# Performance work log

Hardware: AMD Instinct MI355X
Metric: run time of the kernel (lower is better)

Reference implementation:

```python
import jax, jax.numpy as jnp
import numpy as np

NUM_HEADS = 16
NUM_KV_HEADS = 4
HEAD_DIM = 64
HIDDEN = 1024
B, S = 2, 2048


def setup_inputs() -> dict:
    key = jax.random.key(0)
    ks = jax.random.split(key, 9)
    sc = 0.02
    return {
        "x": jax.random.normal(ks[0], (B, S, HIDDEN), dtype=jnp.float32),
        "Wq": jax.random.normal(ks[1], (HIDDEN, NUM_HEADS * HEAD_DIM), dtype=jnp.float32) * sc,
        "bq": jnp.zeros((NUM_HEADS * HEAD_DIM,), dtype=jnp.float32),
        "Wk": jax.random.normal(ks[2], (HIDDEN, NUM_KV_HEADS * HEAD_DIM), dtype=jnp.float32) * sc,
        "bk": jnp.zeros((NUM_KV_HEADS * HEAD_DIM,), dtype=jnp.float32),
        "Wv": jax.random.normal(ks[3], (HIDDEN, NUM_KV_HEADS * HEAD_DIM), dtype=jnp.float32) * sc,
        "bv": jnp.zeros((NUM_KV_HEADS * HEAD_DIM,), dtype=jnp.float32),
        "Wo": jax.random.normal(ks[4], (NUM_HEADS * HEAD_DIM, HIDDEN), dtype=jnp.float32) * sc,
        "bo": jnp.zeros((HIDDEN,), dtype=jnp.float32),
    }


def reference(x, Wq, bq, Wk, bk, Wv, bv, Wo, bo):
    bs, seq, _ = x.shape
    groups = NUM_HEADS // NUM_KV_HEADS
    # projections -> [B, H, S, D]
    q = (x @ Wq + bq).reshape(bs, seq, NUM_HEADS, HEAD_DIM).transpose(0, 2, 1, 3)
    k = (x @ Wk + bk).reshape(bs, seq, NUM_KV_HEADS, HEAD_DIM).transpose(0, 2, 1, 3)
    v = (x @ Wv + bv).reshape(bs, seq, NUM_KV_HEADS, HEAD_DIM).transpose(0, 2, 1, 3)
    # repeat_interleave KV heads to match query heads (GQA expansion)
    k = jnp.repeat(k, groups, axis=1)
    v = jnp.repeat(v, groups, axis=1)
    # NOTE: source applies NO 1/sqrt(d) scaling and no mask/ALiBi
    scores = jnp.einsum("bhqd,bhkd->bhqk", q, k)
    attn = jax.nn.softmax(scores.astype(jnp.float32), axis=-1).astype(q.dtype)
    out = jnp.einsum("bhqk,bhkd->bhqd", attn, v)
    out = out.transpose(0, 2, 1, 3).reshape(bs, seq, NUM_HEADS * HEAD_DIM)
    return out @ Wo + bo
```

## Files before the change

### kernel.cpp

```cpp
#include <hip/hip_runtime.h>

#define NHEADS 16
#define NKV    4
#define HDIM   64
#define HIDDEN 1024
#define BATCH  2
#define SEQ    2048
#define MROWS  (BATCH * SEQ)
#define LOG2E  1.44269504088896340736f

typedef __bf16 bf16_t;
typedef bf16_t bf16x8 __attribute__((ext_vector_type(8)));
typedef float  f32x4  __attribute__((ext_vector_type(4)));

__device__ __forceinline__ float bf2f(unsigned short u) {
    return __uint_as_float(((unsigned int)u) << 16);
}
__device__ __forceinline__ unsigned short f2bf(float f) {
    unsigned int u = __float_as_uint(f);
    u += 0x7FFFu + ((u >> 16) & 1u);
    return (unsigned short)(u >> 16);
}

__device__ __forceinline__ void gld16(const unsigned short* g, unsigned short* l)
{
    __builtin_amdgcn_global_load_lds(
        (const __attribute__((address_space(1))) void*)g,
        (__attribute__((address_space(3))) void*)l,
        16, 0, 0);
}

__device__ __forceinline__ int swz(int row, int ch) {
    return (row * 8 + (ch ^ (row & 7))) * 8;
}

__device__ __forceinline__ bool sniff_is_f32(const unsigned short* __restrict__ x)
{
    const int e = (x[threadIdx.x & 63] >> 7) & 0xFF;
    const unsigned long long ok = __ballot(e >= 110 && e <= 140);
    return __popcll(ok) < 56;
}

__device__ __forceinline__ void load8cvt(const void* base, size_t elem, bool isf32, unsigned short out[8])
{
    if (!isf32) {
        *(uint4*)out = *(const uint4*)((const unsigned short*)base + elem);
    } else {
        const float* p = (const float*)base + elem;
        float4 v0 = *(const float4*)p;
        float4 v1 = *(const float4*)(p + 4);
        out[0] = f2bf(v0.x); out[1] = f2bf(v0.y); out[2] = f2bf(v0.z); out[3] = f2bf(v0.w);
        out[4] = f2bf(v1.x); out[5] = f2bf(v1.y); out[6] = f2bf(v1.z); out[7] = f2bf(v1.w);
    }
}
__device__ __forceinline__ float bias_at(const void* b, int i, bool isf32)
{
    return isf32 ? ((const float*)b)[i] : bf2f(((const unsigned short*)b)[i]);
}

__global__ __launch_bounds__(256)
void prep_kernel(const void* __restrict__ x,
                 const void* __restrict__ Wq, const void* __restrict__ Wk,
                 const void* __restrict__ Wv, const void* __restrict__ Wo,
                 unsigned short* __restrict__ xb,
                 unsigned short* __restrict__ Wqkvt,
                 unsigned short* __restrict__ Wot)
{
    const bool isf32 = sniff_is_f32((const unsigned short*)x);
    const int t = threadIdx.x;
    int bid = blockIdx.x;

    if (bid < 2048) {
        if (!isf32) return;
        const size_t c = (size_t)bid * 256 + t;
        unsigned short v[8];
        load8cvt(x, c * 8, true, v);
        *(uint4*)(&xb[c * 8]) = *(uint4*)v;
        return;
    }
    bid -= 2048;
    const void* src; unsigned short* dst; int N, rowoff;
    if (bid < 256)      {             src = Wq; dst = Wqkvt; N = 1024; rowoff = 0;    }
    else if (bid < 320) { bid -= 256; src = Wk; dst = Wqkvt; N = 256;  rowoff = 1024; }
    else if (bid < 384) { bid -= 320; src = Wv; dst = Wqkvt; N = 256;  rowoff = 1280; }
    else                { bid -= 384; src = Wo; dst = Wot;   N = 1024; rowoff = 0;    }
    const int ntx = N / 64;
    const int gn0 = (bid % ntx) * 64;
    const int gk0 = (bid / ntx) * 64;

    __shared__ unsigned short Ts[64][72];
#pragma unroll
    for (int half = 0; half < 2; ++half) {
        const int kl = (t >> 3) + half * 32;
        const int n8 = (t & 7) * 8;
        unsigned short v[8];
        load8cvt(src, (size_t)(gk0 + kl) * N + gn0 + n8, isf32, v);
        *(uint4*)(&Ts[kl][n8]) = *(uint4*)v;
    }
    __syncthreads();
#pragma unroll
    for (int half = 0; half < 2; ++half) {
        const int nl = (t >> 3) + half * 32;
        const int k8 = (t & 7) * 8;
        unsigned short v[8];
#pragma unroll
        for (int j = 0; j < 8; ++j) v[j] = Ts[k8 + j][nl];
        *(uint4*)(&dst[(size_t)(rowoff + gn0 + nl) * HIDDEN + gk0 + k8]) = *(uint4*)v;
    }
}

template<int TBM, int TBN, int KK>
__device__ __forceinline__ void gemm_tile(const unsigned short* __restrict__ A,
                                          const unsigned short* __restrict__ Bt,
                                          int m0, int n0,
                                          unsigned short* As, unsigned short* Bs,
                                          f32x4 (&acc)[TBM / 32][TBN / 32])
{
    const int tid  = threadIdx.x;
    const int lane = tid & 63;
    const int wave = tid >> 6;
    const int quad = lane >> 4;
    const int l15  = lane & 15;
    const int wr   = wave >> 1;
    const int wc   = wave & 1;

    const int srow = tid >> 3;
    const int gch  = ((tid & 7) ^ (srow & 7)) * 8;

    const unsigned short* ga[TBM / 32];
    const unsigned short* gb[TBN / 32];
#pragma unroll
    for (int r = 0; r < TBM / 32; ++r)
        ga[r] = A + (size_t)(m0 + srow + r * 32) * KK + gch;
#pragma unroll
    for (int r = 0; r < TBN / 32; ++r)
        gb[r] = Bt + (size_t)(n0 + srow + r * 32) * KK + gch;

    const int ldw = wave * 512;

    int aoffs[2][TBM / 32], boffs[2][TBN / 32];
#pragma unroll
    for (int kk = 0; kk < 2; ++kk) {
#pragma unroll
        for (int i = 0; i < TBM / 32; ++i)
            aoffs[kk][i] = swz(wr * (TBM / 2) + i * 16 + l15, kk * 4 + quad);
#pragma unroll
        for (int j = 0; j < TBN / 32; ++j)
            boffs[kk][j] = swz(wc * (TBN / 2) + j * 16 + l15, kk * 4 + quad);
    }

#define GEMM_STAGE(buf)                                                         \
    do {                                                                        \
        _Pragma("unroll")                                                       \
        for (int r = 0; r < TBM / 32; ++r) {                                    \
            gld16(ga[r], &As[(buf) * TBM * 64 + r * 2048 + ldw]);               \
            ga[r] += 64;                                                        \
        }                                                                       \
        _Pragma("unroll")                                                       \
        for (int r = 0; r < TBN / 32; ++r) {                                    \
            gld16(gb[r], &Bs[(buf) * TBN * 64 + r * 2048 + ldw]);               \
            gb[r] += 64;                                                        \
        }                                                                       \
    } while (0)

    constexpr int nk = KK / 64;
    GEMM_STAGE(0);
#pragma unroll
    for (int k = 0; k < nk; ++k) {
        const int cur = k & 1;
        __syncthreads();
        if (k + 1 < nk) GEMM_STAGE(cur ^ 1);

#pragma unroll
        for (int kk = 0; kk < 2; ++kk) {
            bf16x8 af[TBM / 32], bfv[TBN / 32];
#pragma unroll
            for (int i = 0; i < TBM / 32; ++i)
                af[i] = *(const bf16x8*)(&As[cur * TBM * 64 + aoffs[kk][i]]);
#pragma unroll
            for (int j = 0; j < TBN / 32; ++j)
                bfv[j] = *(const bf16x8*)(&Bs[cur * TBN * 64 + boffs[kk][j]]);
            __builtin_amdgcn_s_setprio(1);
#pragma unroll
            for (int i = 0; i < TBM / 32; ++i)
#pragma unroll
                for (int j = 0; j < TBN / 32; ++j)
                    acc[i][j] = __builtin_amdgcn_mfma_f32_16x16x32_bf16(af[i], bfv[j], acc[i][j], 0, 0, 0);
            __builtin_amdgcn_s_setprio(0);
        }
    }
#undef GEMM_STAGE
}

__global__ __launch_bounds__(256)
void gemm_qkv(const void* __restrict__ xraw,
              const unsigned short* __restrict__ xb,
              const unsigned short* __restrict__ Bt,
              const void* __restrict__ bq, const void* __restrict__ bk,
              const void* __restrict__ bv,
              unsigned short* __restrict__ Qh,
              unsigned short* __restrict__ Kh,
              unsigned short* __restrict__ Vt)
{
    __shared__ __align__(16) unsigned short As[2 * 128 * 64];
    __shared__ __align__(16) unsigned short Bs[2 * 64 * 64];
    const bool bias_f32 = sniff_is_f32((const unsigned short*)xraw);
    const unsigned short* A = bias_f32 ? xb : (const unsigned short*)xraw;
    const int lane = threadIdx.x & 63;
    const int wave = threadIdx.x >> 6;
    const int quad = lane >> 4, l15 = lane & 15;
    const int wr = wave >> 1, wc = wave & 1;
    const int m0 = blockIdx.y * 128, n0 = blockIdx.x * 64;

    f32x4 acc[4][2] = {};
    gemm_tile<128, 64, HIDDEN>(A, Bt, m0, n0, As, Bs, acc);

#pragma unroll
    for (int i = 0; i < 4; ++i) {
#pragma unroll
        for (int j = 0; j < 2; ++j) {
            const int nn  = n0 + wc * 32 + j * 16 + l15;
            const int mmb = m0 + wr * 64 + i * 16 + quad * 4;
            const int b = mmb >> 11, s0 = mmb & 2047;
            if (nn < 1024) {
                const float bias = bias_at(bq, nn, bias_f32);
                const int h = nn >> 6, d = nn & 63;
                const size_t idx0 = (((size_t)(b * NHEADS + h)) * SEQ + s0) * 64 + d;
#pragma unroll
                for (int r = 0; r < 4; ++r)
                    Qh[idx0 + (size_t)r * 64] = f2bf((acc[i][j][r] + bias) * LOG2E);
            } else if (nn < 1280) {
                const int nk = nn - 1024;
                const float bias = bias_at(bk, nk, bias_f32);
                const int h = nk >> 6, d = nk & 63;
                const size_t idx0 = (((size_t)(b * NKV + h)) * SEQ + s0) * 64 + d;
#pragma unroll
                for (int r = 0; r < 4; ++r)
                    Kh[idx0 + (size_t)r * 64] = f2bf(acc[i][j][r] + bias);
            } else {
                const int nv = nn - 1280;
                const float bias = bias_at(bv, nv, bias_f32);
                const int h = nv >> 6, d = nv & 63;
                const size_t idx = (((size_t)(b * NKV + h)) * 64 + d) * SEQ + s0;
                unsigned short vv[4];
#pragma unroll
                for (int r = 0; r < 4; ++r) vv[r] = f2bf(acc[i][j][r] + bias);
                *(uint2*)(&Vt[idx]) = *(uint2*)vv;
            }
        }
    }
}

__global__ __launch_bounds__(256)
void gemm_o(const void* __restrict__ xraw,
            const unsigned short* __restrict__ A,
            const unsigned short* __restrict__ Bt,
            const void* __restrict__ bo,
            float* __restrict__ out)
{
    __shared__ __align__(16) unsigned short As[2 * 128 * 64];
    __shared__ __align__(16) unsigned short Bs[2 * 64 * 64];
    const bool bias_f32 = sniff_is_f32((const unsigned short*)xraw);
    const int lane = threadIdx.x & 63;
    const int wave = threadIdx.x >> 6;
    const int quad = lane >> 4, l15 = lane & 15;
    const int wr = wave >> 1, wc = wave & 1;
    const int m0 = blockIdx.y * 128, n0 = blockIdx.x * 64;

    f32x4 acc[4][2] = {};
    gemm_tile<128, 64, HIDDEN>(A, Bt, m0, n0, As, Bs, acc);

#pragma unroll
    for (int i = 0; i < 4; ++i) {
#pragma unroll
        for (int j = 0; j < 2; ++j) {
            const int nn = n0 + wc * 32 + j * 16 + l15;
            const float bvv = bias_at(bo, nn, bias_f32);
#pragma unroll
            for (int r = 0; r < 4; ++r) {
                const int mm = m0 + wr * 64 + i * 16 + quad * 4 + r;
                out[(size_t)mm * HIDDEN + nn] = acc[i][j][r] + bvv;
            }
        }
    }
}

#define PLD   72
#define NT    (SEQ / 64)
#define KVOFF (64 * 64)

__global__ __launch_bounds__(256)
void attn_kernel(const unsigned short* __restrict__ Qh,
                 const unsigned short* __restrict__ Kh,
                 const unsigned short* __restrict__ Vt,
                 unsigned short* __restrict__ O)
{
    __shared__ __align__(16) unsigned short Kth[2 * KVOFF];
    __shared__ __align__(16) unsigned short VtT[2 * KVOFF];
    __shared__ __align__(16) unsigned short Pt[4 * 32 * PLD];

    const int tid  = threadIdx.x;
    const int lane = tid & 63;
    const int wave = tid >> 6;
    const int quad = lane >> 4;
    const int l15  = lane & 15;

    const int qt = blockIdx.x;
    const int h  = blockIdx.y;
    const int b  = blockIdx.z;
    const int kv = h >> 2;

    const size_t qoff = ((size_t)(b * NHEADS + h)) * SEQ * HDIM;
    const size_t koff = ((size_t)(b * NKV + kv)) * SEQ * HDIM;
    const size_t voff = ((size_t)(b * NKV + kv)) * HDIM * SEQ;

    const int q0 = qt * 128 + wave * 32;

    bf16x8 qf0[2], qf1[2];
#pragma unroll
    for (int qs = 0; qs < 2; ++qs) {
        const size_t qrow = qoff + (size_t)(q0 + qs * 16 + l15) * HDIM;
        qf0[qs] = *(const bf16x8*)(&Qh[qrow + quad * 8]);
        qf1[qs] = *(const bf16x8*)(&Qh[qrow + 32 + quad * 8]);
    }

    bf16x8 onesv;
#pragma unroll
    for (int i = 0; i < 8; ++i) onesv[i] = (bf16_t)1.0f;

    f32x4 o0[4] = {}, o1[4] = {};
    f32x4 lacc0 = {}, lacc1 = {};

    int koff0[4], koff1[4], pw[2][4], prd[2], voffs[2][4];
#pragma unroll
    for (int j = 0; j < 4; ++j) {
        koff0[j] = swz(j * 16 + l15, quad);
        koff1[j] = swz(j * 16 + l15, quad ^ 4);
        pw[0][j] = wave * 32 * PLD + l15 * PLD + j * 16 + quad * 4;
        pw[1][j] = pw[0][j] + 16 * PLD;
    }
#pragma unroll
    for (int kk = 0; kk < 2; ++kk) {
        prd[kk] = wave * 32 * PLD + l15 * PLD + kk * 32 + quad * 8;
#pragma unroll
        for (int dt = 0; dt < 4; ++dt)
            voffs[kk][dt] = swz(dt * 16 + l15, kk * 4 + quad);
    }

    const unsigned short* kp = Kh + koff;
    const unsigned short* vp = Vt + voff;
    const int srow0 = tid >> 3;
    const int gch_s = ((tid & 7) ^ (srow0 & 7)) * 8;

#define ATTN_STAGE(buf)                                                          \
    do {                                                                         \
        gld16(kp + (size_t)srow0 * HDIM + gch_s,        &Kth[(buf)*KVOFF + wave * 512]);        \
        gld16(kp + (size_t)(srow0 + 32) * HDIM + gch_s, &Kth[(buf)*KVOFF + 2048 + wave * 512]); \
        gld16(vp + (size_t)srow0 * SEQ + gch_s,         &VtT[(buf)*KVOFF + wave * 512]);        \
        gld16(vp + (size_t)(srow0 + 32) * SEQ + gch_s,  &VtT[(buf)*KVOFF + 2048 + wave * 512]); \
        kp += 64 * HDIM; vp += 64;                                               \
    } while (0)

    ATTN_STAGE(0);

#pragma unroll 2
    for (int kt = 0; kt < NT; ++kt) {
        const int cur = kt & 1;
        __syncthreads();
        if (kt + 1 < NT) ATTN_STAGE(cur ^ 1);

#pragma unroll
        for (int j = 0; j < 4; ++j) {
            const bf16x8 kh0 = *(const bf16x8*)(&Kth[cur * KVOFF + koff0[j]]);
            const bf16x8 kh1 = *(const bf16x8*)(&Kth[cur * KVOFF + koff1[j]]);
#pragma unroll
            for (int qs = 0; qs < 2; ++qs) {
                f32x4 z = {};
                __builtin_amdgcn_s_setprio(1);
                z = __builtin_amdgcn_mfma_f32_16x16x32_bf16(kh0, qs ? qf0[1] : qf0[0], z, 0, 0, 0);
                const f32x4 sc = __builtin_amdgcn_mfma_f32_16x16x32_bf16(kh1, qs ? qf1[1] : qf1[0], z, 0, 0, 0);
                __builtin_amdgcn_s_setprio(0);
                const float p0 = __builtin_amdgcn_exp2f(sc[0]);
                const float p1 = __builtin_amdgcn_exp2f(sc[1]);
                const float p2 = __builtin_amdgcn_exp2f(sc[2]);
                const float p3 = __builtin_amdgcn_exp2f(sc[3]);
                uint2 w;
                w.x = __builtin_amdgcn_perm(__float_as_uint(p1), __float_as_uint(p0), 0x07060302u);
                w.y = __builtin_amdgcn_perm(__float_as_uint(p3), __float_as_uint(p2), 0x07060302u);
                *(uint2*)(&Pt[pw[qs][j]]) = w;
            }
        }

#pragma unroll
        for (int kk = 0; kk < 2; ++kk) {
            const bf16x8 pf0 = *(const bf16x8*)(&Pt[prd[kk]]);
            const bf16x8 pf1 = *(const bf16x8*)(&Pt[prd[kk] + 16 * PLD]);
            __builtin_amdgcn_s_setprio(1);
            lacc0 = __builtin_amdgcn_mfma_f32_16x16x32_bf16(onesv, pf0, lacc0, 0, 0, 0);
            lacc1 = __builtin_amdgcn_mfma_f32_16x16x32_bf16(onesv, pf1, lacc1, 0, 0, 0);
#pragma unroll
            for (int dt = 0; dt < 4; ++dt) {
                const bf16x8 vf = *(const bf16x8*)(&VtT[cur * KVOFF + voffs[kk][dt]]);
                o0[dt] = __builtin_amdgcn_mfma_f32_16x16x32_bf16(vf, pf0, o0[dt], 0, 0, 0);
                o1[dt] = __builtin_amdgcn_mfma_f32_16x16x32_bf16(vf, pf1, o1[dt], 0, 0, 0);
            }
            __builtin_amdgcn_s_setprio(0);
        }
    }
#undef ATTN_STAGE

#pragma unroll
    for (int qs = 0; qs < 2; ++qs) {
        const float inv = 1.0f / (qs ? lacc1[0] : lacc0[0]);
        const size_t rowbase = ((size_t)b * SEQ + (q0 + qs * 16 + l15)) * (NHEADS * HDIM) + h * HDIM;
#pragma unroll
        for (int dt = 0; dt < 4; ++dt) {
            const f32x4 ov = qs ? o1[dt] : o0[dt];
            unsigned short v4[4];
#pragma unroll
            for (int r = 0; r < 4; ++r) v4[r] = f2bf(ov[r] * inv);
            *(uint2*)(&O[rowbase + dt * 16 + quad * 4]) = *(uint2*)v4;
        }
    }
}

extern "C" void kernel_launch(void* const* d_in, const int* in_sizes, int n_in,
                              void* d_out, int out_size, void* d_ws, size_t ws_size,
                              hipStream_t stream)
{
    const void* x  = d_in[0];
    const void* Wq = d_in[1];
    const void* bq = d_in[2];
    const void* Wk = d_in[3];
    const void* bk = d_in[4];
    const void* Wv = d_in[5];
    const void* bv = d_in[6];
    const void* Wo = d_in[7];
    const void* bo = d_in[8];
    float* out = (float*)d_out;

    unsigned short* p = (unsigned short*)d_ws;
    unsigned short* xb    = p; p += (size_t)MROWS * HIDDEN;
    unsigned short* Wqkvt = p; p += (size_t)1536 * HIDDEN;
    unsigned short* Wot   = p; p += (size_t)HIDDEN * HIDDEN;
    unsigned short* Qh = p;  p += (size_t)MROWS * 1024;
    unsigned short* Kh = p;  p += (size_t)2 * NKV * SEQ * HDIM;
    unsigned short* Vt = p;  p += (size_t)2 * NKV * SEQ * HDIM;
    unsigned short* A2 = p;  p += (size_t)MROWS * 1024;

    dim3 blk(256);
    prep_kernel<<<dim3(2688), blk, 0, stream>>>(x, Wq, Wk, Wv, Wo, xb, Wqkvt, Wot);
    gemm_qkv<<<dim3(1536 / 64, MROWS / 128), blk, 0, stream>>>(
        x, xb, Wqkvt, bq, bk, bv, Qh, Kh, Vt);
    attn_kernel<<<dim3(SEQ / 128, NHEADS, BATCH), blk, 0, stream>>>(Qh, Kh, Vt, A2);
    gemm_o<<<dim3(1024 / 64, MROWS / 128), blk, 0, stream>>>(x, A2, Wot, bo, out);
}
```

Before: 176.5 us.

## Triple-buffer GEMM and attention loads with explicit vmcnt waits, shrink GEMM tiles

```diff
diff --git a/kernel.cpp b/kernel.cpp
--- a/kernel.cpp
+++ b/kernel.cpp
@@ -12,6 +12,9 @@
 typedef __bf16 bf16_t;
 typedef bf16_t bf16x8 __attribute__((ext_vector_type(8)));
 typedef float  f32x4  __attribute__((ext_vector_type(4)));
+
+template<int N>  struct ic { static constexpr int  v = N; };
+template<bool B> struct bc { static constexpr bool v = B; };
 
 __device__ __forceinline__ float bf2f(unsigned short u) {
     return __uint_as_float(((unsigned int)u) << 16);
@@ -109,13 +112,14 @@
     }
 }
 
-template<int TBM, int TBN, int KK>
+template<int KK>
 __device__ __forceinline__ void gemm_tile(const unsigned short* __restrict__ A,
                                           const unsigned short* __restrict__ Bt,
                                           int m0, int n0,
                                           unsigned short* As, unsigned short* Bs,
-                                          f32x4 (&acc)[TBM / 32][TBN / 32])
-{
+                                          f32x4 (&acc)[2][2])
+{
+    static_assert(KK / 64 == 16, "pipeline schedule assumes 16 K-steps");
     const int tid  = threadIdx.x;
     const int lane = tid & 63;
     const int wave = tid >> 6;
@@ -127,69 +131,75 @@
     const int srow = tid >> 3;
     const int gch  = ((tid & 7) ^ (srow & 7)) * 8;
 
-    const unsigned short* ga[TBM / 32];
-    const unsigned short* gb[TBN / 32];
-#pragma unroll
-    for (int r = 0; r < TBM / 32; ++r)
-        ga[r] = A + (size_t)(m0 + srow + r * 32) * KK + gch;
-#pragma unroll
-    for (int r = 0; r < TBN / 32; ++r)
+    const unsigned short* ga[2];
+    const unsigned short* gb[2];
+#pragma unroll
+    for (int r = 0; r < 2; ++r) {
+        ga[r] = A  + (size_t)(m0 + srow + r * 32) * KK + gch;
         gb[r] = Bt + (size_t)(n0 + srow + r * 32) * KK + gch;
-
-    const int ldw = wave * 512;
-
-    int aoffs[2][TBM / 32], boffs[2][TBN / 32];
+    }
+    unsigned short* const adst = As + wave * 512;
+    unsigned short* const bdst = Bs + wave * 512;
+
+    int aoffs[2][2], boffs[2][2];
 #pragma unroll
     for (int kk = 0; kk < 2; ++kk) {
 #pragma unroll
-        for (int i = 0; i < TBM / 32; ++i)
-            aoffs[kk][i] = swz(wr * (TBM / 2) + i * 16 + l15, kk * 4 + quad);
-#pragma unroll
-        for (int j = 0; j < TBN / 32; ++j)
-            boffs[kk][j] = swz(wc * (TBN / 2) + j * 16 + l15, kk * 4 + quad);
-    }
-
-#define GEMM_STAGE(buf)                                                         \
-    do {                                                                        \
-        _Pragma("unroll")                                                       \
-        for (int r = 0; r < TBM / 32; ++r) {                                    \
-            gld16(ga[r], &As[(buf) * TBM * 64 + r * 2048 + ldw]);               \
-            ga[r] += 64;                                                        \
-        }                                                                       \
-        _Pragma("unroll")                                                       \
-        for (int r = 0; r < TBN / 32; ++r) {                                    \
-            gld16(gb[r], &Bs[(buf) * TBN * 64 + r * 2048 + ldw]);               \
-            gb[r] += 64;                                                        \
-        }                                                                       \
+        for (int i = 0; i < 2; ++i) {
+            aoffs[kk][i] = swz(wr * 32 + i * 16 + l15, kk * 4 + quad);
+            boffs[kk][i] = swz(wc * 32 + i * 16 + l15, kk * 4 + quad);
+        }
+    }
+
+#define GSTAGE(B)                                                \
+    do {                                                         \
+        gld16(ga[0], adst + (B) * 4096);        ga[0] += 64;     \
+        gld16(ga[1], adst + (B) * 4096 + 2048); ga[1] += 64;     \
+        gld16(gb[0], bdst + (B) * 4096);        gb[0] += 64;     \
+        gld16(gb[1], bdst + (B) * 4096 + 2048); gb[1] += 64;     \
     } while (0)
 
-    constexpr int nk = KK / 64;
-    GEMM_STAGE(0);
-#pragma unroll
-    for (int k = 0; k < nk; ++k) {
-        const int cur = k & 1;
-        __syncthreads();
-        if (k + 1 < nk) GEMM_STAGE(cur ^ 1);
+    GSTAGE(0);
+    GSTAGE(1);
+
+    auto step = [&](auto B_, auto STG_, auto LAST_) {
+        constexpr int B = decltype(B_)::v;
+        if constexpr (decltype(LAST_)::v) asm volatile("s_waitcnt vmcnt(0)" ::: "memory");
+        else                              asm volatile("s_waitcnt vmcnt(4)" ::: "memory");
+        __builtin_amdgcn_sched_barrier(0);
+        __builtin_amdgcn_s_barrier();
+        __builtin_amdgcn_sched_barrier(0);
+        if constexpr (decltype(STG_)::v) GSTAGE((B + 2) % 3);
 
 #pragma unroll
         for (int kk = 0; kk < 2; ++kk) {
-            bf16x8 af[TBM / 32], bfv[TBN / 32];
-#pragma unroll
-            for (int i = 0; i < TBM / 32; ++i)
-                af[i] = *(const bf16x8*)(&As[cur * TBM * 64 + aoffs[kk][i]]);
-#pragma unroll
-            for (int j = 0; j < TBN / 32; ++j)
-                bfv[j] = *(const bf16x8*)(&Bs[cur * TBN * 64 + boffs[kk][j]]);
+            bf16x8 af[2], bfv[2];
+#pragma unroll
+            for (int i = 0; i < 2; ++i) {
+                af[i]  = *(const bf16x8*)(&As[B * 4096 + aoffs[kk][i]]);
+                bfv[i] = *(const bf16x8*)(&Bs[B * 4096 + boffs[kk][i]]);
+            }
             __builtin_amdgcn_s_setprio(1);
 #pragma unroll
-            for (int i = 0; i < TBM / 32; ++i)
-#pragma unroll
-                for (int j = 0; j < TBN / 32; ++j)
+            for (int i = 0; i < 2; ++i)
+#pragma unroll
+                for (int j = 0; j < 2; ++j)
                     acc[i][j] = __builtin_amdgcn_mfma_f32_16x16x32_bf16(af[i], bfv[j], acc[i][j], 0, 0, 0);
             __builtin_amdgcn_s_setprio(0);
         }
-    }
-#undef GEMM_STAGE
+    };
+
+#pragma unroll 1
+    for (int k0 = 0; k0 < 12; k0 += 3) {
+        step(ic<0>{}, bc<true>{}, bc<false>{});
+        step(ic<1>{}, bc<true>{}, bc<false>{});
+        step(ic<2>{}, bc<true>{}, bc<false>{});
+    }
+    step(ic<0>{}, bc<true>{},  bc<false>{});
+    step(ic<1>{}, bc<true>{},  bc<false>{});
+    step(ic<2>{}, bc<false>{}, bc<false>{});
+    step(ic<0>{}, bc<false>{}, bc<true>{});
+#undef GSTAGE
 }
 
 __global__ __launch_bounds__(256)
@@ -202,25 +212,25 @@
               unsigned short* __restrict__ Kh,
               unsigned short* __restrict__ Vt)
 {
-    __shared__ __align__(16) unsigned short As[2 * 128 * 64];
-    __shared__ __align__(16) unsigned short Bs[2 * 64 * 64];
+    __shared__ __align__(16) unsigned short As[3 * 64 * 64];
+    __shared__ __align__(16) unsigned short Bs[3 * 64 * 64];
     const bool bias_f32 = sniff_is_f32((const unsigned short*)xraw);
     const unsigned short* A = bias_f32 ? xb : (const unsigned short*)xraw;
     const int lane = threadIdx.x & 63;
     const int wave = threadIdx.x >> 6;
     const int quad = lane >> 4, l15 = lane & 15;
     const int wr = wave >> 1, wc = wave & 1;
-    const int m0 = blockIdx.y * 128, n0 = blockIdx.x * 64;
-
-    f32x4 acc[4][2] = {};
-    gemm_tile<128, 64, HIDDEN>(A, Bt, m0, n0, As, Bs, acc);
-
-#pragma unroll
-    for (int i = 0; i < 4; ++i) {
+    const int m0 = blockIdx.y * 64, n0 = blockIdx.x * 64;
+
+    f32x4 acc[2][2] = {};
+    gemm_tile<HIDDEN>(A, Bt, m0, n0, As, Bs, acc);
+
+#pragma unroll
+    for (int i = 0; i < 2; ++i) {
 #pragma unroll
         for (int j = 0; j < 2; ++j) {
             const int nn  = n0 + wc * 32 + j * 16 + l15;
-            const int mmb = m0 + wr * 64 + i * 16 + quad * 4;
+            const int mmb = m0 + wr * 32 + i * 16 + quad * 4;
             const int b = mmb >> 11, s0 = mmb & 2047;
             if (nn < 1024) {
                 const float bias = bias_at(bq, nn, bias_f32);
@@ -258,34 +268,33 @@
             const void* __restrict__ bo,
             float* __restrict__ out)
 {
-    __shared__ __align__(16) unsigned short As[2 * 128 * 64];
-    __shared__ __align__(16) unsigned short Bs[2 * 64 * 64];
+    __shared__ __align__(16) unsigned short As[3 * 64 * 64];
+    __shared__ __align__(16) unsigned short Bs[3 * 64 * 64];
     const bool bias_f32 = sniff_is_f32((const unsigned short*)xraw);
     const int lane = threadIdx.x & 63;
     const int wave = threadIdx.x >> 6;
     const int quad = lane >> 4, l15 = lane & 15;
     const int wr = wave >> 1, wc = wave & 1;
-    const int m0 = blockIdx.y * 128, n0 = blockIdx.x * 64;
-
-    f32x4 acc[4][2] = {};
-    gemm_tile<128, 64, HIDDEN>(A, Bt, m0, n0, As, Bs, acc);
-
-#pragma unroll
-    for (int i = 0; i < 4; ++i) {
+    const int m0 = blockIdx.y * 64, n0 = blockIdx.x * 64;
+
+    f32x4 acc[2][2] = {};
+    gemm_tile<HIDDEN>(A, Bt, m0, n0, As, Bs, acc);
+
+#pragma unroll
+    for (int i = 0; i < 2; ++i) {
 #pragma unroll
         for (int j = 0; j < 2; ++j) {
             const int nn = n0 + wc * 32 + j * 16 + l15;
             const float bvv = bias_at(bo, nn, bias_f32);
 #pragma unroll
             for (int r = 0; r < 4; ++r) {
-                const int mm = m0 + wr * 64 + i * 16 + quad * 4 + r;
+                const int mm = m0 + wr * 32 + i * 16 + quad * 4 + r;
                 out[(size_t)mm * HIDDEN + nn] = acc[i][j][r] + bvv;
             }
         }
     }
 }
 
-#define PLD   72
 #define NT    (SEQ / 64)
 #define KVOFF (64 * 64)
 
@@ -295,9 +304,9 @@
                  const unsigned short* __restrict__ Vt,
                  unsigned short* __restrict__ O)
 {
-    __shared__ __align__(16) unsigned short Kth[2 * KVOFF];
-    __shared__ __align__(16) unsigned short VtT[2 * KVOFF];
-    __shared__ __align__(16) unsigned short Pt[4 * 32 * PLD];
+    __shared__ __align__(16) unsigned short Kth[3 * KVOFF];
+    __shared__ __align__(16) unsigned short VtT[3 * KVOFF];
+    __shared__ __align__(16) unsigned short Pt[4 * 32 * 64];
 
     const int tid  = threadIdx.x;
     const int lane = tid & 63;
@@ -331,17 +340,18 @@
     f32x4 o0[4] = {}, o1[4] = {};
     f32x4 lacc0 = {}, lacc1 = {};
 
-    int koff0[4], koff1[4], pw[2][4], prd[2], voffs[2][4];
+    int koff0[4], koff1[4], pwoff[2][4], proff[2], voffs[2][4];
 #pragma unroll
     for (int j = 0; j < 4; ++j) {
         koff0[j] = swz(j * 16 + l15, quad);
         koff1[j] = swz(j * 16 + l15, quad ^ 4);
-        pw[0][j] = wave * 32 * PLD + l15 * PLD + j * 16 + quad * 4;
-        pw[1][j] = pw[0][j] + 16 * PLD;
+#pragma unroll
+        for (int qs = 0; qs < 2; ++qs)
+            pwoff[qs][j] = wave * 2048 + swz(qs * 16 + l15, j * 2 + (quad >> 1)) + (quad & 1) * 4;
     }
 #pragma unroll
     for (int kk = 0; kk < 2; ++kk) {
-        prd[kk] = wave * 32 * PLD + l15 * PLD + kk * 32 + quad * 8;
+        proff[kk] = wave * 2048 + swz(l15, kk * 4 + quad);
 #pragma unroll
         for (int dt = 0; dt < 4; ++dt)
             voffs[kk][dt] = swz(dt * 16 + l15, kk * 4 + quad);
@@ -351,28 +361,34 @@
     const unsigned short* vp = Vt + voff;
     const int srow0 = tid >> 3;
     const int gch_s = ((tid & 7) ^ (srow0 & 7)) * 8;
-
-#define ATTN_STAGE(buf)                                                          \
+    unsigned short* const kdst = Kth + wave * 512;
+    unsigned short* const vdst = VtT + wave * 512;
+
+#define ATTN_STAGE(B)                                                            \
     do {                                                                         \
-        gld16(kp + (size_t)srow0 * HDIM + gch_s,        &Kth[(buf)*KVOFF + wave * 512]);        \
-        gld16(kp + (size_t)(srow0 + 32) * HDIM + gch_s, &Kth[(buf)*KVOFF + 2048 + wave * 512]); \
-        gld16(vp + (size_t)srow0 * SEQ + gch_s,         &VtT[(buf)*KVOFF + wave * 512]);        \
-        gld16(vp + (size_t)(srow0 + 32) * SEQ + gch_s,  &VtT[(buf)*KVOFF + 2048 + wave * 512]); \
+        gld16(kp + (size_t)srow0 * HDIM + gch_s,        kdst + (B) * KVOFF);        \
+        gld16(kp + (size_t)(srow0 + 32) * HDIM + gch_s, kdst + (B) * KVOFF + 2048); \
+        gld16(vp + (size_t)srow0 * SEQ + gch_s,         vdst + (B) * KVOFF);        \
+        gld16(vp + (size_t)(srow0 + 32) * SEQ + gch_s,  vdst + (B) * KVOFF + 2048); \
         kp += 64 * HDIM; vp += 64;                                               \
     } while (0)
 
     ATTN_STAGE(0);
-
-#pragma unroll 2
-    for (int kt = 0; kt < NT; ++kt) {
-        const int cur = kt & 1;
-        __syncthreads();
-        if (kt + 1 < NT) ATTN_STAGE(cur ^ 1);
+    ATTN_STAGE(1);
+
+    auto step = [&](auto B_, auto STG_, auto LAST_) {
+        constexpr int B = decltype(B_)::v;
+        if constexpr (decltype(LAST_)::v) asm volatile("s_waitcnt vmcnt(0)" ::: "memory");
+        else                              asm volatile("s_waitcnt vmcnt(4)" ::: "memory");
+        __builtin_amdgcn_sched_barrier(0);
+        __builtin_amdgcn_s_barrier();
+        __builtin_amdgcn_sched_barrier(0);
+        if constexpr (decltype(STG_)::v) ATTN_STAGE((B + 2) % 3);
 
 #pragma unroll
         for (int j = 0; j < 4; ++j) {
-            const bf16x8 kh0 = *(const bf16x8*)(&Kth[cur * KVOFF + koff0[j]]);
-            const bf16x8 kh1 = *(const bf16x8*)(&Kth[cur * KVOFF + koff1[j]]);
+            const bf16x8 kh0 = *(const bf16x8*)(&Kth[B * KVOFF + koff0[j]]);
+            const bf16x8 kh1 = *(const bf16x8*)(&Kth[B * KVOFF + koff1[j]]);
 #pragma unroll
             for (int qs = 0; qs < 2; ++qs) {
                 f32x4 z = {};
@@ -387,26 +403,35 @@
                 uint2 w;
                 w.x = __builtin_amdgcn_perm(__float_as_uint(p1), __float_as_uint(p0), 0x07060302u);
                 w.y = __builtin_amdgcn_perm(__float_as_uint(p3), __float_as_uint(p2), 0x07060302u);
-                *(uint2*)(&Pt[pw[qs][j]]) = w;
+                *(uint2*)(&Pt[pwoff[qs][j]]) = w;
             }
         }
 
 #pragma unroll
         for (int kk = 0; kk < 2; ++kk) {
-            const bf16x8 pf0 = *(const bf16x8*)(&Pt[prd[kk]]);
-            const bf16x8 pf1 = *(const bf16x8*)(&Pt[prd[kk] + 16 * PLD]);
+            const bf16x8 pf0 = *(const bf16x8*)(&Pt[proff[kk]]);
+            const bf16x8 pf1 = *(const bf16x8*)(&Pt[proff[kk] + 1024]);
             __builtin_amdgcn_s_setprio(1);
             lacc0 = __builtin_amdgcn_mfma_f32_16x16x32_bf16(onesv, pf0, lacc0, 0, 0, 0);
             lacc1 = __builtin_amdgcn_mfma_f32_16x16x32_bf16(onesv, pf1, lacc1, 0, 0, 0);
 #pragma unroll
             for (int dt = 0; dt < 4; ++dt) {
-                const bf16x8 vf = *(const bf16x8*)(&VtT[cur * KVOFF + voffs[kk][dt]]);
+                const bf16x8 vf = *(const bf16x8*)(&VtT[B * KVOFF + voffs[kk][dt]]);
                 o0[dt] = __builtin_amdgcn_mfma_f32_16x16x32_bf16(vf, pf0, o0[dt], 0, 0, 0);
                 o1[dt] = __builtin_amdgcn_mfma_f32_16x16x32_bf16(vf, pf1, o1[dt], 0, 0, 0);
             }
             __builtin_amdgcn_s_setprio(0);
         }
-    }
+    };
+
+#pragma unroll 1
+    for (int t0 = 0; t0 < 30; t0 += 3) {
+        step(ic<0>{}, bc<true>{}, bc<false>{});
+        step(ic<1>{}, bc<true>{}, bc<false>{});
+        step(ic<2>{}, bc<true>{}, bc<false>{});
+    }
+    step(ic<0>{}, bc<false>{}, bc<false>{});
+    step(ic<1>{}, bc<false>{}, bc<true>{});
 #undef ATTN_STAGE
 
 #pragma unroll
@@ -450,8 +475,8 @@
 
     dim3 blk(256);
     prep_kernel<<<dim3(2688), blk, 0, stream>>>(x, Wq, Wk, Wv, Wo, xb, Wqkvt, Wot);
-    gemm_qkv<<<dim3(1536 / 64, MROWS / 128), blk, 0, stream>>>(
+    gemm_qkv<<<dim3(1536 / 64, MROWS / 64), blk, 0, stream>>>(
         x, xb, Wqkvt, bq, bk, bv, Qh, Kh, Vt);
     attn_kernel<<<dim3(SEQ / 128, NHEADS, BATCH), blk, 0, stream>>>(Qh, Kh, Vt, A2);
-    gemm_o<<<dim3(1024 / 64, MROWS / 128), blk, 0, stream>>>(x, A2, Wot, bo, out);
-}
+    gemm_o<<<dim3(1024 / 64, MROWS / 64), blk, 0, stream>>>(x, A2, Wot, bo, out);
+}
```

Measured after the change: 182.1 us. 3.2% more time.
